# Kernel optimization log

Measured on AMD Instinct MI355X. Metric: run time of the kernel, lower is better.

## Reference

```python
import jax, jax.numpy as jnp
import numpy as np

MESH = 4194304

def setup_inputs() -> dict:
    key = jax.random.key(0)
    k1, k2 = jax.random.split(key)
    theta_t = jax.random.normal(k1, (MESH - 1,), dtype=jnp.float32) * 0.01
    state = jax.random.normal(k2, (MESH, 2), dtype=jnp.float32)
    # SSH eigenstates are unit vectors
    state = state / jnp.linalg.norm(state, axis=-1, keepdims=True)
    return {"theta_t": theta_t, "state": state}

def reference(theta_t, state):
    M = state.shape[0]
    # --- deformation: deformed[0]=state[0]; deformed[i+1] = R(theta[i]) @ state[i+1]
    c, s = jnp.cos(theta_t), jnp.sin(theta_t)            # (M-1,)
    sx, sy = state[1:, 0], state[1:, 1]
    rot = jnp.stack([c * sx - s * sy, s * sx + c * sy], axis=-1)  # (M-1, 2)
    deformed = jnp.concatenate([state[:1], rot], axis=0)          # (M, 2)
    # --- neighbor overlaps (periodic): dots[i] = d_i . d_{i+1}, dots[M-1] = d_{M-1} . d_0
    dots = jnp.sum(deformed * jnp.roll(deformed, -1, axis=0), axis=-1)  # (M,)
    vols = jnp.sqrt(jnp.abs(1.0 - jnp.abs(dots) ** 2))                   # (M,)
    loss_v = jnp.sum(vols)
    loss_s = jnp.sum(vols ** 2)
    # --- dirichlet / SO(2) smoothness loss; average_length uses vol_loss.item() (stop-grad)
    avg_len = jnp.abs(jax.lax.stop_gradient(loss_v) / M)
    sim = jnp.exp(-vols / avg_len)                       # used for i = 0 .. M-2
    # note: original wrap-around similarity has NO sqrt (faithful to source)
    sim_last = jnp.exp(-(1.0 - jnp.abs(dots[-1]) ** 2) / avg_len)
    loss_so2 = (jnp.abs(theta_t[0]) * sim[0]
                + jnp.abs(theta_t[-1]) * sim_last
                + jnp.sum(jnp.abs(theta_t[:-1] - theta_t[1:]) * sim[1:M - 1]))
    # total loss with ratio = ratio_s = 1.0
    return loss_v + loss_so2 + loss_s
```

## Files before the change

### kernel.cpp

```cpp
#include <hip/hip_runtime.h>
#include <math.h>

#define MESH 4194304
#define NBLOCKS 2048
#define NTHREADS 256
#define KPT 8
#define STRIDE (NBLOCKS * NTHREADS)

__device__ __forceinline__ float2 rot2(float t, float2 v) {
  float s, c;
  __sincosf(t, &s, &c);
  return make_float2(c * v.x - s * v.y, s * v.x + c * v.y);
}

__device__ __forceinline__ float block_reduce(float v, float* red) {
  #pragma unroll
  for (int off = 32; off > 0; off >>= 1) v += __shfl_down(v, off);
  const int lane = threadIdx.x & 63, wid = threadIdx.x >> 6;
  if (lane == 0) red[wid] = v;
  __syncthreads();
  return red[0] + red[1] + red[2] + red[3];
}

__global__ void passA_kernel(const float* __restrict__ theta,
                             const float2* __restrict__ state,
                             float2* __restrict__ pv) {
  const int tid0 = blockIdx.x * NTHREADS + threadIdx.x;
  float th_a[KPT], th_b[KPT];
  float2 st_a[KPT], st_b[KPT];
  #pragma unroll
  for (int k = 0; k < KPT; ++k) {
    const int i = tid0 + k * STRIDE;
    const int ip1 = (i + 1 == MESH) ? 0 : i + 1;
    th_a[k] = (i == 0) ? 0.f : theta[i - 1];
    th_b[k] = (ip1 == 0) ? 0.f : theta[ip1 - 1];
    st_a[k] = state[i];
    st_b[k] = state[ip1];
  }
  float lv = 0.f, ls = 0.f;
  #pragma unroll
  for (int k = 0; k < KPT; ++k) {
    const float2 a = rot2(th_a[k], st_a[k]);
    const float2 b = rot2(th_b[k], st_b[k]);
    const float dot = a.x * b.x + a.y * b.y;
    const float v2 = fabsf(1.f - dot * dot);
    lv += sqrtf(v2);
    ls += v2;
  }
  __shared__ float red1[4], red2[4];
  const float blv = block_reduce(lv, red1);
  const float bls = block_reduce(ls, red2);
  if (threadIdx.x == 0) pv[blockIdx.x] = make_float2(blv, bls);
}

__global__ void reduceA_kernel(const float2* __restrict__ pv,
                               double* __restrict__ acc,
                               float* __restrict__ inv_avg) {
  double lv = 0.0, ls = 0.0;
  for (int i = threadIdx.x; i < NBLOCKS; i += 1024) {
    const float2 p = pv[i];
    lv += (double)p.x;
    ls += (double)p.y;
  }
  #pragma unroll
  for (int off = 32; off > 0; off >>= 1) {
    lv += __shfl_down(lv, off);
    ls += __shfl_down(ls, off);
  }
  __shared__ double s1[16], s2[16];
  const int lane = threadIdx.x & 63, wid = threadIdx.x >> 6;
  if (lane == 0) { s1[wid] = lv; s2[wid] = ls; }
  __syncthreads();
  if (threadIdx.x == 0) {
    double tlv = 0.0, tls = 0.0;
    #pragma unroll
    for (int w = 0; w < 16; ++w) { tlv += s1[w]; tls += s2[w]; }
    acc[0] = tlv + tls;
    *inv_avg = (float)((double)MESH / fabs(tlv));
  }
}

__global__ void passC_kernel(const float* __restrict__ theta,
                             const float2* __restrict__ state,
                             const float* __restrict__ inv_avg_p,
                             float* __restrict__ pl) {
  const float inv_avg = *inv_avg_p;
  const int tid0 = blockIdx.x * NTHREADS + threadIdx.x;
  float th_a[KPT], th_b[KPT];
  float2 st_a[KPT], st_b[KPT];
  #pragma unroll
  for (int k = 0; k < KPT; ++k) {
    const int i = tid0 + k * STRIDE;
    const int ip1 = (i + 1 == MESH) ? 0 : i + 1;
    th_a[k] = (i == 0) ? 0.f : theta[i - 1];
    th_b[k] = (ip1 == 0) ? 0.f : theta[ip1 - 1];
    st_a[k] = state[i];
    st_b[k] = state[ip1];
  }
  float lso = 0.f;
  #pragma unroll
  for (int k = 0; k < KPT; ++k) {
    const int i = tid0 + k * STRIDE;
    const float2 a = rot2(th_a[k], st_a[k]);
    const float2 b = rot2(th_b[k], st_b[k]);
    const float dot = a.x * b.x + a.y * b.y;
    const float v2s = 1.f - dot * dot;
    const float w = fabsf(th_a[k] - th_b[k]);
    const float earg = (i == MESH - 1) ? v2s : sqrtf(fabsf(v2s));
    lso += w * __expf(-earg * inv_avg);
  }
  __shared__ float red1[4];
  const float blso = block_reduce(lso, red1);
  if (threadIdx.x == 0) pl[blockIdx.x] = blso;
}

__global__ void reduceC_kernel(const float* __restrict__ pl,
                               const double* __restrict__ acc,
                               float* __restrict__ out) {
  double lso = 0.0;
  for (int i = threadIdx.x; i < NBLOCKS; i += 1024) lso += (double)pl[i];
  #pragma unroll
  for (int off = 32; off > 0; off >>= 1) lso += __shfl_down(lso, off);
  __shared__ double s1[16];
  const int lane = threadIdx.x & 63, wid = threadIdx.x >> 6;
  if (lane == 0) s1[wid] = lso;
  __syncthreads();
  if (threadIdx.x == 0) {
    double t = 0.0;
    #pragma unroll
    for (int w = 0; w < 16; ++w) t += s1[w];
    out[0] = (float)(acc[0] + t);
  }
}

extern "C" void kernel_launch(void* const* d_in, const int* in_sizes, int n_in,
                              void* d_out, int out_size, void* d_ws, size_t ws_size,
                              hipStream_t stream) {
  const float* theta  = (const float*)d_in[0];
  const float2* state = (const float2*)d_in[1];
  float* out = (float*)d_out;

  char* ws = (char*)d_ws;
  float2* pv = (float2*)ws;
  float* pl = (float*)(ws + 16384);
  double* acc = (double*)(ws + 24576);
  float* inv_avg = (float*)(ws + 24576 + 16);

  passA_kernel<<<NBLOCKS, NTHREADS, 0, stream>>>(theta, state, pv);
  reduceA_kernel<<<1, 1024, 0, stream>>>(pv, acc, inv_avg);
  passC_kernel<<<NBLOCKS, NTHREADS, 0, stream>>>(theta, state, inv_avg, pl);
  reduceC_kernel<<<1, 1024, 0, stream>>>(pl, acc, out);
}
```

Measured before the change: 102.3 us.

## Load contiguous float4 chunks per lane and exchange neighbors via wave shuffles

Restructures both passes so that each wave handles a contiguous 512-element segment. Each lane loads four consecutive theta and state values as float4 vectors, and neighbor values come from wave shuffles instead of a second, unaligned global load. This removes the duplicated and misaligned reads (state[i+1], theta[i-1]) and uses wider memory transactions. The cost is more complicated boundary handling across lanes, groups and waves, plus special cases at the mesh end, which adds correctness risk.

```diff
diff --git a/kernel.cpp b/kernel.cpp
--- a/kernel.cpp
+++ b/kernel.cpp
@@ -4,13 +4,12 @@
 #define MESH 4194304
 #define NBLOCKS 2048
 #define NTHREADS 256
-#define KPT 8
-#define STRIDE (NBLOCKS * NTHREADS)
+#define QPG 2
 
-__device__ __forceinline__ float2 rot2(float t, float2 v) {
+__device__ __forceinline__ float2 rot2(float t, float x, float y) {
   float s, c;
   __sincosf(t, &s, &c);
-  return make_float2(c * v.x - s * v.y, s * v.x + c * v.y);
+  return make_float2(c * x - s * y, s * x + c * y);
 }
 
 __device__ __forceinline__ float block_reduce(float v, float* red) {
@@ -22,35 +21,86 @@
   return red[0] + red[1] + red[2] + red[3];
 }
 
-__global__ void passA_kernel(const float* __restrict__ theta,
-                             const float2* __restrict__ state,
-                             float2* __restrict__ pv) {
-  const int tid0 = blockIdx.x * NTHREADS + threadIdx.x;
-  float th_a[KPT], th_b[KPT];
-  float2 st_a[KPT], st_b[KPT];
+template <bool PASS_C>
+__global__ void pass_kernel(const float* __restrict__ theta,
+                            const float* __restrict__ statef,
+                            const float* __restrict__ inv_avg_p,
+                            float2* __restrict__ pv,
+                            float* __restrict__ pl) {
+  const int tid = threadIdx.x;
+  const int lane = tid & 63, wid = tid >> 6;
+  const int wbase = (blockIdx.x * 4 + wid) << 9;
+
+  float4 tf[QPG], sA[QPG], sB[QPG];
   #pragma unroll
-  for (int k = 0; k < KPT; ++k) {
-    const int i = tid0 + k * STRIDE;
-    const int ip1 = (i + 1 == MESH) ? 0 : i + 1;
-    th_a[k] = (i == 0) ? 0.f : theta[i - 1];
-    th_b[k] = (ip1 == 0) ? 0.f : theta[ip1 - 1];
-    st_a[k] = state[i];
-    st_b[k] = state[ip1];
+  for (int g = 0; g < QPG; ++g) {
+    const int e0 = wbase + (g << 8) + (lane << 2);
+    if (e0 != MESH - 4) {
+      tf[g] = *(const float4*)(theta + e0);
+    } else {
+      tf[g] = make_float4(theta[e0], theta[e0 + 1], theta[e0 + 2], 0.f);
+    }
+    sA[g] = *(const float4*)(statef + 2 * e0);
+    sB[g] = *(const float4*)(statef + 2 * e0 + 4);
   }
-  float lv = 0.f, ls = 0.f;
+  float th_carry = 0.f;
+  if (lane == 0 && wbase > 0) th_carry = theta[wbase - 1];
+  float2 s_carry = make_float2(0.f, 0.f);
+  if (lane == 63) {
+    const int en = (wbase + 512 == MESH) ? 0 : wbase + 512;
+    s_carry = make_float2(statef[2 * en], statef[2 * en + 1]);
+  }
+  const float inv_avg = PASS_C ? *inv_avg_p : 0.f;
+
+  float acc0 = 0.f, acc1 = 0.f;
   #pragma unroll
-  for (int k = 0; k < KPT; ++k) {
-    const float2 a = rot2(th_a[k], st_a[k]);
-    const float2 b = rot2(th_b[k], st_b[k]);
-    const float dot = a.x * b.x + a.y * b.y;
-    const float v2 = fabsf(1.f - dot * dot);
-    lv += sqrtf(v2);
-    ls += v2;
+  for (int g = 0; g < QPG; ++g) {
+    const int e0 = wbase + (g << 8) + (lane << 2);
+    const float prevw = (g == 0) ? th_carry : __shfl(tf[g - 1].w, 63);
+    float th0 = __shfl_up(tf[g].w, 1);
+    if (lane == 0) th0 = prevw;
+    const float bx = (g + 1 < QPG) ? __shfl(sA[g + 1].x, 0) : s_carry.x;
+    const float by = (g + 1 < QPG) ? __shfl(sA[g + 1].y, 0) : s_carry.y;
+    float nx = __shfl_down(sA[g].x, 1);
+    float ny = __shfl_down(sA[g].y, 1);
+    if (lane == 63) { nx = bx; ny = by; }
+
+    const float2 d0 = rot2(th0,     sA[g].x, sA[g].y);
+    const float2 d1 = rot2(tf[g].x, sA[g].z, sA[g].w);
+    const float2 d2 = rot2(tf[g].y, sB[g].x, sB[g].y);
+    const float2 d3 = rot2(tf[g].z, sB[g].z, sB[g].w);
+    const float2 d4 = rot2(tf[g].w, nx, ny);
+
+    const float dots[4] = {d0.x * d1.x + d0.y * d1.y, d1.x * d2.x + d1.y * d2.y,
+                           d2.x * d3.x + d2.y * d3.y, d3.x * d4.x + d3.y * d4.y};
+    if (!PASS_C) {
+      #pragma unroll
+      for (int j = 0; j < 4; ++j) {
+        const float v2 = fabsf(1.f - dots[j] * dots[j]);
+        acc0 += sqrtf(v2);
+        acc1 += v2;
+      }
+    } else {
+      const float thseq[5] = {th0, tf[g].x, tf[g].y, tf[g].z, tf[g].w};
+      #pragma unroll
+      for (int j = 0; j < 4; ++j) {
+        const float v2s = 1.f - dots[j] * dots[j];
+        const float w = fabsf(thseq[j] - thseq[j + 1]);
+        const float earg = (e0 == MESH - 4 && j == 3) ? v2s : sqrtf(fabsf(v2s));
+        acc0 += w * __expf(-earg * inv_avg);
+      }
+    }
   }
+
   __shared__ float red1[4], red2[4];
-  const float blv = block_reduce(lv, red1);
-  const float bls = block_reduce(ls, red2);
-  if (threadIdx.x == 0) pv[blockIdx.x] = make_float2(blv, bls);
+  if (!PASS_C) {
+    const float b0 = block_reduce(acc0, red1);
+    const float b1 = block_reduce(acc1, red2);
+    if (tid == 0) pv[blockIdx.x] = make_float2(b0, b1);
+  } else {
+    const float b0 = block_reduce(acc0, red1);
+    if (tid == 0) pl[blockIdx.x] = b0;
+  }
 }
 
 __global__ void reduceA_kernel(const float2* __restrict__ pv,
@@ -80,40 +130,6 @@
   }
 }
 
-__global__ void passC_kernel(const float* __restrict__ theta,
-                             const float2* __restrict__ state,
-                             const float* __restrict__ inv_avg_p,
-                             float* __restrict__ pl) {
-  const float inv_avg = *inv_avg_p;
-  const int tid0 = blockIdx.x * NTHREADS + threadIdx.x;
-  float th_a[KPT], th_b[KPT];
-  float2 st_a[KPT], st_b[KPT];
-  #pragma unroll
-  for (int k = 0; k < KPT; ++k) {
-    const int i = tid0 + k * STRIDE;
-    const int ip1 = (i + 1 == MESH) ? 0 : i + 1;
-    th_a[k] = (i == 0) ? 0.f : theta[i - 1];
-    th_b[k] = (ip1 == 0) ? 0.f : theta[ip1 - 1];
-    st_a[k] = state[i];
-    st_b[k] = state[ip1];
-  }
-  float lso = 0.f;
-  #pragma unroll
-  for (int k = 0; k < KPT; ++k) {
-    const int i = tid0 + k * STRIDE;
-    const float2 a = rot2(th_a[k], st_a[k]);
-    const float2 b = rot2(th_b[k], st_b[k]);
-    const float dot = a.x * b.x + a.y * b.y;
-    const float v2s = 1.f - dot * dot;
-    const float w = fabsf(th_a[k] - th_b[k]);
-    const float earg = (i == MESH - 1) ? v2s : sqrtf(fabsf(v2s));
-    lso += w * __expf(-earg * inv_avg);
-  }
-  __shared__ float red1[4];
-  const float blso = block_reduce(lso, red1);
-  if (threadIdx.x == 0) pl[blockIdx.x] = blso;
-}
-
 __global__ void reduceC_kernel(const float* __restrict__ pl,
                                const double* __restrict__ acc,
                                float* __restrict__ out) {
@@ -137,7 +153,7 @@
                               void* d_out, int out_size, void* d_ws, size_t ws_size,
                               hipStream_t stream) {
   const float* theta  = (const float*)d_in[0];
-  const float2* state = (const float2*)d_in[1];
+  const float* statef = (const float*)d_in[1];
   float* out = (float*)d_out;
 
   char* ws = (char*)d_ws;
@@ -146,8 +162,8 @@
   double* acc = (double*)(ws + 24576);
   float* inv_avg = (float*)(ws + 24576 + 16);
 
-  passA_kernel<<<NBLOCKS, NTHREADS, 0, stream>>>(theta, state, pv);
+  pass_kernel<false><<<NBLOCKS, NTHREADS, 0, stream>>>(theta, statef, inv_avg, pv, pl);
   reduceA_kernel<<<1, 1024, 0, stream>>>(pv, acc, inv_avg);
-  passC_kernel<<<NBLOCKS, NTHREADS, 0, stream>>>(theta, state, inv_avg, pl);
+  pass_kernel<true><<<NBLOCKS, NTHREADS, 0, stream>>>(theta, statef, inv_avg, pv, pl);
   reduceC_kernel<<<1, 1024, 0, stream>>>(pl, acc, out);
 }
```

After: 98.00 us. -4.2%, faster.
